# Kernel optimization log

Hardware: AMD Instinct MI355X
Metric: run time of the kernel (lower is better)

Reference implementation:

```python
import jax, jax.numpy as jnp
import numpy as np

D_MODEL = 1024
N_HEADS = 16
HEAD_DIM = D_MODEL // N_HEADS
SEQ_LEN = 2048
D_FF = 4 * D_MODEL
LCC_SCALE = 0.1
LN_EPS = 1e-5
NORM_EPS = 1e-12  # F.normalize eps


def _layer_norm(x, g, b):
    mu = jnp.mean(x, axis=-1, keepdims=True)
    var = jnp.mean(jnp.square(x - mu), axis=-1, keepdims=True)
    return (x - mu) * jax.lax.rsqrt(var + LN_EPS) * g + b


def setup_inputs() -> dict:
    key = jax.random.key(0)
    ks = jax.random.split(key, 8)
    s = 0.02  # weight init scale
    return {
        "x": jax.random.normal(ks[0], (SEQ_LEN, D_MODEL), jnp.float32),
        "lcc_values": jax.random.uniform(ks[1], (SEQ_LEN,), jnp.float32),
        "w_qkv": jax.random.normal(ks[2], (D_MODEL, 3 * D_MODEL), jnp.float32) * s,
        "b_qkv": jnp.zeros((3 * D_MODEL,), jnp.float32),
        "w_out": jax.random.normal(ks[3], (D_MODEL, D_MODEL), jnp.float32) * s,
        "b_out": jnp.zeros((D_MODEL,), jnp.float32),
        "ln1_g": jnp.ones((D_MODEL,), jnp.float32),
        "ln1_b": jnp.zeros((D_MODEL,), jnp.float32),
        "ln2_g": jnp.ones((D_MODEL,), jnp.float32),
        "ln2_b": jnp.zeros((D_MODEL,), jnp.float32),
        "w_ff1": jax.random.normal(ks[4], (D_MODEL, D_FF), jnp.float32) * s,
        "b_ff1": jnp.zeros((D_FF,), jnp.float32),
        "w_ff2": jax.random.normal(ks[5], (D_FF, D_MODEL), jnp.float32) * s,
        "b_ff2": jnp.zeros((D_MODEL,), jnp.float32),
    }


def reference(x, lcc_values, w_qkv, b_qkv, w_out, b_out, ln1_g, ln1_b,
              ln2_g, ln2_b, w_ff1, b_ff1, w_ff2, b_ff2):
    L = x.shape[0]
    scaling = HEAD_DIM ** -0.5

    normed = _layer_norm(x, ln1_g, ln1_b)
    qkv = normed @ w_qkv + b_qkv                      # [L, 3D]
    qkv = qkv.reshape(L, 3, N_HEADS, HEAD_DIM)
    q = jnp.transpose(qkv[:, 0], (1, 0, 2))           # [H, L, d]
    k = jnp.transpose(qkv[:, 1], (1, 0, 2))
    v = jnp.transpose(qkv[:, 2], (1, 0, 2))

    # cosine attention: L2-normalize q, k
    q = q / jnp.maximum(jnp.linalg.norm(q, axis=-1, keepdims=True), NORM_EPS)
    k = k / jnp.maximum(jnp.linalg.norm(k, axis=-1, keepdims=True), NORM_EPS)
    q = q * scaling

    scores = jnp.einsum('hld,hmd->hlm', q, k)         # [H, L, L]
    bias = (lcc_values[:, None] + lcc_values[None, :]) * 0.5 * LCC_SCALE
    scores = jnp.clip(scores + bias[None], -10.0, 10.0)
    probs = jax.nn.softmax(scores, axis=-1)

    attn = jnp.einsum('hlm,hmd->hld', probs, v)       # [H, L, d]
    attn = jnp.transpose(attn, (1, 0, 2)).reshape(L, D_MODEL)
    x = x + (attn @ w_out + b_out)

    normed2 = _layer_norm(x, ln2_g, ln2_b)
    h = jax.nn.gelu(normed2 @ w_ff1 + b_ff1, approximate=False)
    x = x + (h @ w_ff2 + b_ff2)
    return x
```

## Files before the change

### kernel.cpp

```cpp
#include <hip/hip_runtime.h>
#include <hip/hip_bf16.h>

#define D_MODEL 1024
#define SEQ 2048
#define NH 16
#define HD 64
#define DFF 4096

typedef __attribute__((ext_vector_type(8))) __bf16 bf16x8;
typedef __attribute__((ext_vector_type(4))) float f32x4;

__device__ __forceinline__ unsigned short f2bf(float f) {
    union { float f; unsigned u; } v; v.f = f;
    unsigned r = v.u + 0x7fffu + ((v.u >> 16) & 1u);
    return (unsigned short)(r >> 16);
}
__device__ __forceinline__ unsigned pack2(float a, float b) {
    return (unsigned)f2bf(a) | ((unsigned)f2bf(b) << 16);
}
__device__ __forceinline__ float bf2f(unsigned short u) {
    union { unsigned u; float f; } v; v.u = ((unsigned)u) << 16;
    return v.f;
}
__device__ __forceinline__ bf16x8 ld_frag(const unsigned short* p) {
    union { uint4 u; bf16x8 b; } c;
    c.u = *(const uint4*)p;
    return c.b;
}

typedef __attribute__((address_space(3))) unsigned lds_u32;
typedef const __attribute__((address_space(1))) unsigned glob_u32;
__device__ __forceinline__ void gl_lds16(const unsigned short* g, unsigned short* l) {
    __builtin_amdgcn_global_load_lds((glob_u32*)g, (lds_u32*)l, 16, 0, 0);
}

#define MFMA16(a,b,c) __builtin_amdgcn_mfma_f32_16x16x32_bf16(a,b,c,0,0,0)

__global__ __launch_bounds__(256) void wcast_all(const float* __restrict__ wq, const float* __restrict__ wo,
                                                 const float* __restrict__ wf1, const float* __restrict__ wf2,
                                                 unsigned short* __restrict__ oq, unsigned short* __restrict__ oo,
                                                 unsigned short* __restrict__ of1, unsigned short* __restrict__ of2) {
    __shared__ unsigned short lt[64][72];
    int id = blockIdx.x;
    const float* W; unsigned short* O; int K, N, nb, kb;
    if (id < 768)       { W = wq;  O = oq;  K = 1024; N = 3072; nb = id % 48; kb = id / 48; }
    else if (id < 1024) { id -= 768;  W = wo;  O = oo;  K = 1024; N = 1024; nb = id & 15; kb = id >> 4; }
    else if (id < 2048) { id -= 1024; W = wf1; O = of1; K = 1024; N = 4096; nb = id & 63; kb = id >> 6; }
    else                { id -= 2048; W = wf2; O = of2; K = 4096; N = 1024; nb = id & 15; kb = id >> 4; }
    int t = threadIdx.x;
    int r = t >> 2, c0 = (t & 3) << 4;
    const float* src = W + (size_t)(kb*64 + r) * N + nb*64 + c0;
    float4 f0 = ((const float4*)src)[0];
    float4 f1 = ((const float4*)src)[1];
    float4 f2 = ((const float4*)src)[2];
    float4 f3 = ((const float4*)src)[3];
    unsigned* dst = (unsigned*)&lt[r][c0];
    dst[0]=pack2(f0.x,f0.y); dst[1]=pack2(f0.z,f0.w);
    dst[2]=pack2(f1.x,f1.y); dst[3]=pack2(f1.z,f1.w);
    dst[4]=pack2(f2.x,f2.y); dst[5]=pack2(f2.z,f2.w);
    dst[6]=pack2(f3.x,f3.y); dst[7]=pack2(f3.z,f3.w);
    __syncthreads();
    int n_ = t >> 2, k0 = (t & 3) << 4;
    unsigned obuf[8];
#pragma unroll
    for (int i = 0; i < 8; i++)
        obuf[i] = (unsigned)lt[k0 + 2*i][n_] | ((unsigned)lt[k0 + 2*i + 1][n_] << 16);
    unsigned short* out = O + (size_t)(nb*64 + n_) * K + kb*64 + k0;
    ((uint4*)out)[0] = *(uint4*)&obuf[0];
    ((uint4*)out)[1] = *(uint4*)&obuf[4];
}

__global__ __launch_bounds__(256) void ln_kernel(const float* __restrict__ x,
                                                 const float* __restrict__ g,
                                                 const float* __restrict__ b,
                                                 unsigned short* __restrict__ out) {
    int row = blockIdx.x, t = threadIdx.x;
    float4 v = ((const float4*)(x + (size_t)row * D_MODEL))[t];
    float s  = v.x + v.y + v.z + v.w;
    float sq = v.x*v.x + v.y*v.y + v.z*v.z + v.w*v.w;
#pragma unroll
    for (int m = 1; m < 64; m <<= 1) { s += __shfl_xor(s, m, 64); sq += __shfl_xor(sq, m, 64); }
    __shared__ float ls[4], lq[4];
    int wave = t >> 6, lane = t & 63;
    if (lane == 0) { ls[wave] = s; lq[wave] = sq; }
    __syncthreads();
    s  = ls[0]+ls[1]+ls[2]+ls[3];
    sq = lq[0]+lq[1]+lq[2]+lq[3];
    float mu  = s * (1.0f / D_MODEL);
    float var = sq * (1.0f / D_MODEL) - mu * mu;
    float rs  = rsqrtf(var + 1e-5f);
    int c = t * 4;
    float y0 = (v.x - mu) * rs * g[c+0] + b[c+0];
    float y1 = (v.y - mu) * rs * g[c+1] + b[c+1];
    float y2 = (v.z - mu) * rs * g[c+2] + b[c+2];
    float y3 = (v.w - mu) * rs * g[c+3] + b[c+3];
    unsigned* o = (unsigned*)(out + (size_t)row * D_MODEL + c);
    o[0] = pack2(y0, y1); o[1] = pack2(y2, y3);
}

__global__ __launch_bounds__(256) void reduce_ln(const float* __restrict__ x,
                                                 const float* __restrict__ bout,
                                                 const unsigned short* __restrict__ parts,
                                                 const float* __restrict__ g,
                                                 const float* __restrict__ b,
                                                 float* __restrict__ x1,
                                                 unsigned short* __restrict__ x2n) {
    int row = blockIdx.x, t = threadIdx.x;
    int i = row * 256 + t;
    float4 v = ((const float4*)x)[i];
    float4 bb = ((const float4*)bout)[t];
    v.x += bb.x; v.y += bb.y; v.z += bb.z; v.w += bb.w;
#pragma unroll
    for (int p = 0; p < 4; p++) {
        ushort4 u = ((const ushort4*)(parts + (size_t)p * SEQ * D_MODEL))[i];
        v.x += bf2f(u.x); v.y += bf2f(u.y); v.z += bf2f(u.z); v.w += bf2f(u.w);
    }
    ((float4*)x1)[i] = v;
    float s  = v.x + v.y + v.z + v.w;
    float sq = v.x*v.x + v.y*v.y + v.z*v.z + v.w*v.w;
#pragma unroll
    for (int m = 1; m < 64; m <<= 1) { s += __shfl_xor(s, m, 64); sq += __shfl_xor(sq, m, 64); }
    __shared__ float ls[4], lq[4];
    int wave = t >> 6, lane = t & 63;
    if (lane == 0) { ls[wave] = s; lq[wave] = sq; }
    __syncthreads();
    s  = ls[0]+ls[1]+ls[2]+ls[3];
    sq = lq[0]+lq[1]+lq[2]+lq[3];
    float mu  = s * (1.0f / D_MODEL);
    float var = sq * (1.0f / D_MODEL) - mu * mu;
    float rs  = rsqrtf(var + 1e-5f);
    int c = t * 4;
    float y0 = (v.x - mu) * rs * g[c+0] + b[c+0];
    float y1 = (v.y - mu) * rs * g[c+1] + b[c+1];
    float y2 = (v.z - mu) * rs * g[c+2] + b[c+2];
    float y3 = (v.w - mu) * rs * g[c+3] + b[c+3];
    unsigned* o = (unsigned*)(x2n + (size_t)row * D_MODEL + c);
    o[0] = pack2(y0, y1); o[1] = pack2(y2, y3);
}

__global__ __launch_bounds__(256) void reduce_ff2(const float* __restrict__ res,
                                                  const float* __restrict__ bias,
                                                  const unsigned short* __restrict__ parts,
                                                  float* __restrict__ out) {
    int i = blockIdx.x * 256 + threadIdx.x;
    float4 r = ((const float4*)res)[i];
    float4 b = ((const float4*)bias)[i & (D_MODEL/4 - 1)];
    r.x += b.x; r.y += b.y; r.z += b.z; r.w += b.w;
#pragma unroll
    for (int p = 0; p < 4; p++) {
        ushort4 u = ((const ushort4*)(parts + (size_t)p * SEQ * D_MODEL))[i];
        r.x += bf2f(u.x); r.y += bf2f(u.y); r.z += bf2f(u.z); r.w += bf2f(u.w);
    }
    ((float4*)out)[i] = r;
}

#define BMf 128
#define BNf 256
#define FBUF_U16 ((BMf + BNf) * 64)
#define FSMEM_U16 (2 * FBUF_U16)
__device__ __forceinline__ void gemm_core_ff(const unsigned short* __restrict__ A,
                                             const unsigned short* __restrict__ Bt,
                                             int K, int K0, int KS, int bm, int bn,
                                             unsigned short* smem, f32x4 acc[4][4],
                                             int w, int lane) {
    int quad = lane >> 4, lr = lane & 15;
    int wm = w >> 2, wn = w & 3;
    const unsigned short* pa[2]; int da[2];
#pragma unroll
    for (int i = 0; i < 2; i++) {
        int rl = w*16 + i*8 + (lane >> 3);
        int sc = (lane & 7) ^ (rl & 7);
        pa[i] = A + (size_t)(bm*BMf + rl) * K + K0 + sc*8;
        da[i] = (w*16 + i*8) * 64;
    }
    const unsigned short* pb[4]; int db[4];
#pragma unroll
    for (int i = 0; i < 4; i++) {
        int rl = w*32 + i*8 + (lane >> 3);
        int sc = (lane & 7) ^ (rl & 7);
        pb[i] = Bt + (size_t)(bn*BNf + rl) * K + K0 + sc*8;
        db[i] = BMf*64 + (w*32 + i*8) * 64;
    }
    int foA[2][4], foB[2][4];
#pragma unroll
    for (int i = 0; i < 4; i++) {
        int ra = wm*64 + i*16 + lr;
        foA[0][i] = ra*64 + ((quad     ^ (ra & 7)))*8;
        foA[1][i] = ra*64 + (((quad+4) ^ (ra & 7)))*8;
        int rb = wn*64 + i*16 + lr;
        foB[0][i] = BMf*64 + rb*64 + ((quad     ^ (rb & 7)))*8;
        foB[1][i] = BMf*64 + rb*64 + (((quad+4) ^ (rb & 7)))*8;
    }
    int T = KS >> 6;
#pragma unroll
    for (int t = 0; t < 2; t++) {
        unsigned short* s = smem + t * FBUF_U16;
#pragma unroll
        for (int i = 0; i < 2; i++) gl_lds16(pa[i] + t*64, s + da[i]);
#pragma unroll
        for (int i = 0; i < 4; i++) gl_lds16(pb[i] + t*64, s + db[i]);
    }
    for (int t = 0; t < T; t++) {
        if (t + 1 < T) asm volatile("s_waitcnt vmcnt(6)" ::: "memory");
        else           asm volatile("s_waitcnt vmcnt(0)" ::: "memory");
        __builtin_amdgcn_s_barrier();
        const unsigned short* s = smem + (t & 1) * FBUF_U16;
#pragma unroll
        for (int h = 0; h < 2; h++) {
            bf16x8 af[4], bfr[4];
#pragma unroll
            for (int i = 0; i < 4; i++) af[i]  = ld_frag(s + foA[h][i]);
#pragma unroll
            for (int j = 0; j < 4; j++) bfr[j] = ld_frag(s + foB[h][j]);
            __builtin_amdgcn_s_setprio(1);
#pragma unroll
            for (int i = 0; i < 4; i++)
#pragma unroll
                for (int j = 0; j < 4; j++)
                    acc[i][j] = MFMA16(af[i], bfr[j], acc[i][j]);
            __builtin_amdgcn_s_setprio(0);
        }
        __builtin_amdgcn_s_barrier();
        if (t + 2 < T) {
            unsigned short* sn = smem + (t & 1) * FBUF_U16;
#pragma unroll
            for (int i = 0; i < 2; i++) gl_lds16(pa[i] + (t+2)*64, sn + da[i]);
#pragma unroll
            for (int i = 0; i < 4; i++) gl_lds16(pb[i] + (t+2)*64, sn + db[i]);
        }
    }
}

__device__ __forceinline__ void acc_init(f32x4 acc[4][4]) {
    f32x4 z = {0.f, 0.f, 0.f, 0.f};
#pragma unroll
    for (int i = 0; i < 4; i++)
#pragma unroll
        for (int j = 0; j < 4; j++) acc[i][j] = z;
}

__global__ __launch_bounds__(512, 2) void k_gemm_ff1(const unsigned short* __restrict__ A,
                                                     const unsigned short* __restrict__ Bt,
                                                     const float* __restrict__ bias,
                                                     unsigned short* __restrict__ C,
                                                     int M, int N, int K) {
    __shared__ unsigned short smem[FSMEM_U16];
    int t = threadIdx.x, w = t >> 6, lane = t & 63;
    int bn = blockIdx.x, bm = blockIdx.y;
    int quad = lane >> 4, lr = lane & 15;
    f32x4 acc[4][4];
    acc_init(acc);
    gemm_core_ff(A, Bt, K, 0, K, bm, bn, smem, acc, w, lane);
    int wm = w >> 2, wn = w & 3;
#pragma unroll
    for (int j = 0; j < 4; j++) {
        int col = bn*BNf + wn*64 + j*16 + lr;
        float bvv = bias[col];
#pragma unroll
        for (int i = 0; i < 4; i++) {
            int row0 = bm*BMf + wm*64 + i*16 + quad*4;
#pragma unroll
            for (int r = 0; r < 4; r++) {
                float v = acc[i][j][r] + bvv;
                v = 0.5f * v * (1.0f + erff(v * 0.70710678118654752f));
                C[(size_t)(row0 + r) * N + col] = f2bf(v);
            }
        }
    }
}

__global__ __launch_bounds__(512, 2) void k_gemm_ff2(const unsigned short* __restrict__ A,
                                                     const unsigned short* __restrict__ Bt,
                                                     unsigned short* __restrict__ C,
                                                     int M, int N, int K) {
    __shared__ unsigned short smem[FSMEM_U16];
    int t = threadIdx.x, w = t >> 6, lane = t & 63;
    int bn = blockIdx.x, bm = blockIdx.y, kz = blockIdx.z;
    int quad = lane >> 4, lr = lane & 15;
    int KS = K >> 2;
    f32x4 acc[4][4];
    acc_init(acc);
    gemm_core_ff(A, Bt, K, kz*KS, KS, bm, bn, smem, acc, w, lane);
    int wm = w >> 2, wn = w & 3;
    unsigned short* P = C + (size_t)kz * M * N;
#pragma unroll
    for (int j = 0; j < 4; j++) {
        int col = bn*BNf + wn*64 + j*16 + lr;
#pragma unroll
        for (int i = 0; i < 4; i++) {
            int row0 = bm*BMf + wm*64 + i*16 + quad*4;
#pragma unroll
            for (int r = 0; r < 4; r++)
                P[(size_t)(row0 + r) * N + col] = f2bf(acc[i][j][r]);
        }
    }
}

#define TMg 128
#define TNg 128
#define HALFg ((TMg + TNg) * 64)
#define SMEM_U16 (2 * HALFg)
__device__ __forceinline__ void gemm_core512(const unsigned short* __restrict__ A,
                                             const unsigned short* __restrict__ Bt,
                                             int K, int K0, int KS, int bm, int bn,
                                             unsigned short* smem, f32x4 acc[4][4],
                                             int w, int lane) {
    int quad = lane >> 4, lr = lane & 15;
    int kg = w >> 2;
    const unsigned short* pa[2]; const unsigned short* pb[2];
    int aoff[2], boff[2];
#pragma unroll
    for (int i = 0; i < 2; i++) {
        int rl = i*64 + w*8 + (lane >> 3);
        int sc = (lane & 7) ^ (rl & 7);
        pa[i] = A  + (size_t)(bm*TMg + rl) * K + K0 + sc*8;
        pb[i] = Bt + (size_t)(bn*TNg + rl) * K + K0 + sc*8;
        aoff[i] = (i*64 + w*8) * 64;
        boff[i] = TMg*64 + (i*64 + w*8) * 64;
    }
    int wr = ((w >> 1) & 1) * 64, wc = (w & 1) * 64;
    int foA[4], foB[4];
#pragma unroll
    for (int i = 0; i < 4; i++) {
        int ra = wr + i*16 + lr;
        foA[i] = ra*64 + (((quad + 4*kg) ^ (ra & 7)))*8;
        int rb = wc + i*16 + lr;
        foB[i] = TMg*64 + rb*64 + (((quad + 4*kg) ^ (rb & 7)))*8;
    }
#pragma unroll
    for (int i = 0; i < 2; i++) { gl_lds16(pa[i], smem + aoff[i]); gl_lds16(pb[i], smem + boff[i]); }
    int bo = 0;
    int T = KS >> 6;
    for (int t = 0; t < T; t++) {
        __syncthreads();
        if (t + 1 < T) {
            int nb = bo ^ HALFg;
#pragma unroll
            for (int i = 0; i < 2; i++) {
                gl_lds16(pa[i] + (t+1)*64, smem + nb + aoff[i]);
                gl_lds16(pb[i] + (t+1)*64, smem + nb + boff[i]);
            }
        }
        const unsigned short* s = smem + bo;
        bf16x8 af[4], bfr[4];
#pragma unroll
        for (int i = 0; i < 4; i++) af[i] = ld_frag(s + foA[i]);
#pragma unroll
        for (int j = 0; j < 4; j++) bfr[j] = ld_frag(s + foB[j]);
        __builtin_amdgcn_s_setprio(1);
#pragma unroll
        for (int i = 0; i < 4; i++)
#pragma unroll
            for (int j = 0; j < 4; j++)
                acc[i][j] = MFMA16(af[i], bfr[j], acc[i][j]);
        __builtin_amdgcn_s_setprio(0);
        bo ^= HALFg;
    }
}

__device__ __forceinline__ void acc_merge_split(unsigned short* smem, f32x4 acc[4][4],
                                                int w, int lane) {
    float* X = (float*)smem;
    int kg = w >> 2, p = w & 3, quad = lane >> 4, lr = lane & 15;
    if (kg) {
#pragma unroll
        for (int i = 0; i < 4; i++) {
            f32x4 t0 = acc[i][0]; acc[i][0] = acc[i][2]; acc[i][2] = t0;
            f32x4 t1 = acc[i][1]; acc[i][1] = acc[i][3]; acc[i][3] = t1;
        }
    }
    __syncthreads();
    int g = (kg ^ 1) * 2;
#pragma unroll
    for (int i = 0; i < 4; i++)
#pragma unroll
        for (int r = 0; r < 4; r++) {
            int ro = (i*16 + r*4 + quad)*16 + lr;
            X[(p*4 + g    )*1024 + ro] = acc[i][2][r];
            X[(p*4 + g + 1)*1024 + ro] = acc[i][3][r];
        }
    __syncthreads();
    int k = kg * 2;
#pragma unroll
    for (int i = 0; i < 4; i++)
#pragma unroll
        for (int r = 0; r < 4; r++) {
            int ro = (i*16 + r*4 + quad)*16 + lr;
            acc[i][0][r] += X[(p*4 + k    )*1024 + ro];
            acc[i][1][r] += X[(p*4 + k + 1)*1024 + ro];
        }
}

__global__ __launch_bounds__(512, 4) void k_gemm_qkv(const unsigned short* __restrict__ A,
                                                     const unsigned short* __restrict__ Bt,
                                                     const float* __restrict__ bias,
                                                     unsigned short* __restrict__ qn,
                                                     unsigned short* __restrict__ kn,
                                                     unsigned short* __restrict__ vt) {
    __shared__ unsigned short smem[SMEM_U16];
    int t = threadIdx.x;
    int bn = blockIdx.x, bm = blockIdx.y;
    int w = t >> 6, lane = t & 63;
    int quad = lane >> 4, lr = lane & 15;
    f32x4 acc[4][4];
    acc_init(acc);
    gemm_core512(A, Bt, 1024, 0, 1024, bm, bn, smem, acc, w, lane);

    float* X = (float*)smem;
    int kg = w >> 2, p = w & 3;
    __syncthreads();
    if (kg == 1) {
#pragma unroll
        for (int j = 0; j < 4; j++) {
            float* slot = X + (p*4 + j)*1024;
#pragma unroll
            for (int i = 0; i < 4; i++)
#pragma unroll
                for (int r = 0; r < 4; r++)
                    slot[(i*16 + r*4 + quad)*16 + lr] = acc[i][j][r];
        }
    }
    __syncthreads();
    int wr = ((w >> 1) & 1) * 64, wc = (w & 1) * 64;
    int sec = bn >> 3, hp = bn & 7;
    if (kg == 0) {
#pragma unroll
        for (int j = 0; j < 4; j++) {
            const float* slot = X + (p*4 + j)*1024;
            float bv = bias[bn*TNg + wc + j*16 + lr];
#pragma unroll
            for (int i = 0; i < 4; i++)
#pragma unroll
                for (int r = 0; r < 4; r++)
                    acc[i][j][r] += slot[(i*16 + r*4 + quad)*16 + lr] + bv;
        }
    }

    if (sec < 2) {
        if (kg == 0) {
            int h = hp*2 + (w & 1);
            unsigned short* dst = (sec == 0) ? qn : kn;
            float mul = (sec == 0) ? 0.125f : 1.0f;
#pragma unroll
            for (int i = 0; i < 4; i++)
#pragma unroll
                for (int r = 0; r < 4; r++) {
                    float ss = 0.f;
#pragma unroll
                    for (int j = 0; j < 4; j++) ss += acc[i][j][r]*acc[i][j][r];
                    ss += __shfl_xor(ss, 1, 64); ss += __shfl_xor(ss, 2, 64);
                    ss += __shfl_xor(ss, 4, 64); ss += __shfl_xor(ss, 8, 64);
                    float scale = mul / fmaxf(sqrtf(ss), 1e-12f);
                    int row = bm*TMg + wr + i*16 + quad*4 + r;
                    size_t base = ((size_t)h*SEQ + row) * HD;
#pragma unroll
                    for (int j = 0; j < 4; j++)
                        dst[base + j*16 + lr] = f2bf(acc[i][j][r] * scale);
                }
        }
    } else {
        __syncthreads();
        unsigned short (*lv)[136] = (unsigned short (*)[136])smem;
        if (kg == 0) {
#pragma unroll
            for (int i = 0; i < 4; i++)
#pragma unroll
                for (int j = 0; j < 4; j++)
#pragma unroll
                    for (int r = 0; r < 4; r++)
                        lv[wc + j*16 + lr][wr + i*16 + quad*4 + r] = f2bf(acc[i][j][r]);
        }
        __syncthreads();
        int d = t >> 2, l0 = (t & 3) * 32;
        unsigned short* ov = vt + ((size_t)(hp*128 + d)) * SEQ + bm*TMg + l0;
#pragma unroll
        for (int c = 0; c < 4; c++)
            ((uint4*)ov)[c] = *(uint4*)&lv[d][l0 + c*8];
    }
}

template<int SPLITK>
__device__ __forceinline__ void gemm_part512(const unsigned short* A, const unsigned short* Bt,
                                             unsigned short* C, int M, int N, int K) {
    __shared__ unsigned short smem[SMEM_U16];
    int t = threadIdx.x;
    int bn = blockIdx.x, bm = blockIdx.y, kz = blockIdx.z;
    int w = t >> 6, lane = t & 63;
    int quad = lane >> 4, lr = lane & 15;
    int KS = K / SPLITK;
    f32x4 acc[4][4];
    acc_init(acc);
    gemm_core512(A, Bt, K, kz*KS, KS, bm, bn, smem, acc, w, lane);
    acc_merge_split(smem, acc, w, lane);
    int kg = w >> 2, wr = ((w >> 1) & 1) * 64, wc = (w & 1) * 64;
    unsigned short* P = C + (size_t)kz * M * N;
    int col0 = bn*TNg + wc + (kg*2)*16 + lr;
    int col1 = col0 + 16;
#pragma unroll
    for (int i = 0; i < 4; i++) {
        int row0 = bm*TMg + wr + i*16 + quad*4;
#pragma unroll
        for (int r = 0; r < 4; r++) {
            P[(size_t)(row0 + r) * N + col0] = f2bf(acc[i][0][r]);
            P[(size_t)(row0 + r) * N + col1] = f2bf(acc[i][1][r]);
        }
    }
}
__global__ __launch_bounds__(512, 4) void k_gemm_op(const unsigned short* A, const unsigned short* Bt,
                                                    unsigned short* C, int M, int N, int K) {
    gemm_part512<4>(A, Bt, C, M, N, K);
}

#define KSPLIT 2
#define KTILES (SEQ / 64 / KSPLIT)
__global__ __launch_bounds__(256) void attn_kernel(const unsigned short* __restrict__ qn,
                                                   const unsigned short* __restrict__ kn,
                                                   const unsigned short* __restrict__ vt,
                                                   const float* __restrict__ lcc,
                                                   float* __restrict__ num_ws,
                                                   float* __restrict__ den_ws) {
    __shared__ unsigned short lQP[64*64];
    __shared__ unsigned short lK[2][64*64];
    __shared__ unsigned short lV[2][64*64];
    int h = blockIdx.x, qb = blockIdx.y, kz = blockIdx.z;
    int t = threadIdx.x;
    int wave = t >> 6, lane = t & 63, quad = lane >> 4, lr = lane & 15;
    int r0 = lane >> 3;
    int ch = lane & 7;

    const unsigned short* kn0 = kn + (size_t)h*SEQ*HD + (size_t)kz*(SEQ/KSPLIT)*HD;
    const unsigned short* vt0 = vt + (size_t)h*HD*SEQ + kz*(SEQ/KSPLIT);
    const float* lcc0 = lcc + kz*(SEQ/KSPLIT);

#pragma unroll
    for (int i = 0; i < 2; i++) {
        int rl = wave*16 + i*8 + r0;
        int ss = ch ^ (rl & 7);
        gl_lds16(qn + ((size_t)h*SEQ + qb*64 + rl)*HD + ss*8, lQP + (wave*16 + i*8)*64);
        gl_lds16(kn0 + (size_t)rl*HD + ss*8,                  lK[0] + (wave*16 + i*8)*64);
        gl_lds16(vt0 + (size_t)rl*SEQ + ss*8,                 lV[0] + (wave*16 + i*8)*64);
    }
    __syncthreads();

    bf16x8 aq0 = ld_frag(lQP + (wave*16 + lr)*64 + ((quad     ^ (lr & 7)))*8);
    bf16x8 aq1 = ld_frag(lQP + (wave*16 + lr)*64 + (((quad+4) ^ (lr & 7)))*8);

    f32x4 z = {0.f, 0.f, 0.f, 0.f};
    f32x4 oacc[4]; oacc[0]=z; oacc[1]=z; oacc[2]=z; oacc[3]=z;
    float den[4] = {0.f, 0.f, 0.f, 0.f};

    int cur = 0;
    for (int kb = 0; kb < KTILES; kb++) {
        if (kb + 1 < KTILES) {
            int nxt = cur ^ 1;
#pragma unroll
            for (int i = 0; i < 2; i++) {
                int rl = wave*16 + i*8 + r0;
                int ss = ch ^ (rl & 7);
                gl_lds16(kn0 + (size_t)(kb+1)*64*HD + (size_t)rl*HD + ss*8,
                         lK[nxt] + (wave*16 + i*8)*64);
                gl_lds16(vt0 + (size_t)rl*SEQ + (kb+1)*64 + ss*8,
                         lV[nxt] + (wave*16 + i*8)*64);
            }
        }
        float lmv[4];
#pragma unroll
        for (int j = 0; j < 4; j++) lmv[j] = 0.05f * lcc0[kb*64 + j*16 + lr];

        __builtin_amdgcn_s_setprio(1);
        const unsigned short* Kc = lK[cur];
#pragma unroll
        for (int j = 0; j < 4; j++) {
            bf16x8 b0 = ld_frag(Kc + (j*16 + lr)*64 + ((quad     ^ (lr & 7)))*8);
            bf16x8 b1 = ld_frag(Kc + (j*16 + lr)*64 + (((quad+4) ^ (lr & 7)))*8);
            f32x4 s = z;
            s = MFMA16(aq0, b0, s);
            s = MFMA16(aq1, b1, s);
#pragma unroll
            for (int r = 0; r < 4; r++) {
                float p = __expf(s[r] + lmv[j]);
                den[r] += p;
                int prow = wave*16 + quad*4 + r;
                lQP[prow*64 + (((2*j + (lr >> 3)) ^ (prow & 7)))*8 + (lr & 7)] = f2bf(p);
            }
        }
        bf16x8 ap0 = ld_frag(lQP + (wave*16 + lr)*64 + ((quad     ^ (lr & 7)))*8);
        bf16x8 ap1 = ld_frag(lQP + (wave*16 + lr)*64 + (((quad+4) ^ (lr & 7)))*8);
        const unsigned short* Vc = lV[cur];
#pragma unroll
        for (int j2 = 0; j2 < 4; j2++) {
            bf16x8 b0 = ld_frag(Vc + (j2*16 + lr)*64 + ((quad     ^ (lr & 7)))*8);
            bf16x8 b1 = ld_frag(Vc + (j2*16 + lr)*64 + (((quad+4) ^ (lr & 7)))*8);
            oacc[j2] = MFMA16(ap0, b0, oacc[j2]);
            oacc[j2] = MFMA16(ap1, b1, oacc[j2]);
        }
        __builtin_amdgcn_s_setprio(0);
        __syncthreads();
        cur ^= 1;
    }
#pragma unroll
    for (int r = 0; r < 4; r++)
#pragma unroll
        for (int m = 1; m < 16; m <<= 1) den[r] += __shfl_xor(den[r], m, 64);

    float* nump = num_ws + (((size_t)(h*32 + qb)) * KSPLIT + kz) * 4096;
#pragma unroll
    for (int j2 = 0; j2 < 4; j2++)
#pragma unroll
        for (int r = 0; r < 4; r++)
            nump[(wave*16 + quad*4 + r) * 64 + j2*16 + lr] = oacc[j2][r];
    if (lr == 0) {
        float* denp = den_ws + (((size_t)(h*32 + qb)) * KSPLIT + kz) * 64;
#pragma unroll
        for (int r = 0; r < 4; r++) denp[wave*16 + quad*4 + r] = den[r];
    }
}

__global__ __launch_bounds__(256) void attn_comb(const float* __restrict__ num_ws,
                                                 const float* __restrict__ den_ws,
                                                 unsigned short* __restrict__ attn) {
    int hq = blockIdx.x;
    int h = hq >> 5, qb = hq & 31;
    int t = threadIdx.x;
    int row = t >> 2, col0 = (t & 3) << 4;
    const float* n0 = num_ws + ((size_t)hq * KSPLIT) * 4096 + row*64 + col0;
    const float* n1 = n0 + 4096;
    float d = den_ws[(size_t)hq * KSPLIT * 64 + row] + den_ws[((size_t)hq * KSPLIT + 1) * 64 + row];
    float inv = 1.0f / d;
    unsigned ob[8];
#pragma unroll
    for (int i = 0; i < 4; i++) {
        float4 a = ((const float4*)n0)[i];
        float4 b = ((const float4*)n1)[i];
        ob[2*i]   = pack2((a.x + b.x) * inv, (a.y + b.y) * inv);
        ob[2*i+1] = pack2((a.z + b.z) * inv, (a.w + b.w) * inv);
    }
    unsigned short* op = attn + (size_t)(qb*64 + row) * D_MODEL + h*64 + col0;
    ((uint4*)op)[0] = *(uint4*)&ob[0];
    ((uint4*)op)[1] = *(uint4*)&ob[4];
}

extern "C" void kernel_launch(void* const* d_in, const int* in_sizes, int n_in,
                              void* d_out, int out_size, void* d_ws, size_t ws_size,
                              hipStream_t stream) {
    const float* x      = (const float*)d_in[0];
    const float* lcc    = (const float*)d_in[1];
    const float* w_qkv  = (const float*)d_in[2];
    const float* b_qkv  = (const float*)d_in[3];
    const float* w_out  = (const float*)d_in[4];
    const float* b_out  = (const float*)d_in[5];
    const float* ln1_g  = (const float*)d_in[6];
    const float* ln1_b  = (const float*)d_in[7];
    const float* ln2_g  = (const float*)d_in[8];
    const float* ln2_b  = (const float*)d_in[9];
    const float* w_ff1  = (const float*)d_in[10];
    const float* b_ff1  = (const float*)d_in[11];
    const float* w_ff2  = (const float*)d_in[12];
    const float* b_ff2  = (const float*)d_in[13];

    char* ws = (char*)d_ws;
    unsigned short* wtq  = (unsigned short*)(ws);
    unsigned short* wto  = (unsigned short*)(ws + 6291456);
    unsigned short* wtf1 = (unsigned short*)(ws + 8388608);
    unsigned short* wtf2 = (unsigned short*)(ws + 16777216);
    unsigned short* xn   = (unsigned short*)(ws + 25165824);
    float*          x1   = (float*)(ws + 29360128);
    float*          numw = (float*)(ws + 29360128);
    float*          denw = (float*)(ws + 46137344);
    unsigned short* hbuf = (unsigned short*)(ws + 37748736);
    unsigned short* pOP  = (unsigned short*)(ws + 37748736);
    unsigned short* qnb  = (unsigned short*)(ws + 54525952);
    unsigned short* knb  = (unsigned short*)(ws + 58720256);
    unsigned short* vtb  = (unsigned short*)(ws + 62914560);
    unsigned short* pFF2 = (unsigned short*)(ws);
    unsigned short* attnb = xn;
    unsigned short* x2n  = qnb;
    float* outp = (float*)d_out;


    wcast_all<<<3072, 256, 0, stream>>>(w_qkv, w_out, w_ff1, w_ff2, wtq, wto, wtf1, wtf2);
    ln_kernel<<<SEQ, 256, 0, stream>>>(x, ln1_g, ln1_b, xn);
    k_gemm_qkv<<<dim3(24, 16), 512, 0, stream>>>(xn, wtq, b_qkv, qnb, knb, vtb);
    attn_kernel<<<dim3(16, 32, KSPLIT), 256, 0, stream>>>(qnb, knb, vtb, lcc, numw, denw);
    attn_comb<<<512, 256, 0, stream>>>(numw, denw, attnb);
    k_gemm_op<<<dim3(8, 16, 4), 512, 0, stream>>>(attnb, wto, pOP, SEQ, 1024, 1024);
    reduce_ln<<<SEQ, 256, 0, stream>>>(x, b_out, pOP, ln2_g, ln2_b, x1, x2n);
    k_gemm_ff1<<<dim3(16, 16), 512, 0, stream>>>(x2n, wtf1, b_ff1, hbuf, SEQ, 4096, 1024);
    k_gemm_ff2<<<dim3(4, 16, 4), 512, 0, stream>>>(hbuf, wtf2, pFF2, SEQ, 1024, 4096);
    reduce_ff2<<<SEQ*D_MODEL/1024, 256, 0, stream>>>(x1, b_ff2, pFF2, outp);
}
```

Baseline: 257.0 us.

## Move QKV and out-proj GEMMs onto the larger 128x256 ff GEMM core

Replaces the 128x128 in-block split-K GEMM core, which merged partial sums through LDS, with the wider gemm_core_ff tile already used for the FF GEMMs, applied to both the QKV and out-projection GEMMs. The QKV epilogue is rewritten for the new warp layout, with one head per wave column for the q/k normalization and a 256-column V transpose through LDS. This cuts the grid sizes in half and removes the LDS reduction step. In exchange there are fewer blocks, 192 and 256, to fill the CUs, and occupancy is lower (2 blocks per CU instead of 4).

```diff
diff --git a/kernel.cpp b/kernel.cpp
--- a/kernel.cpp
+++ b/kernel.cpp
@@ -239,6 +239,97 @@
         for (int j = 0; j < 4; j++) acc[i][j] = z;
 }
 
+__global__ __launch_bounds__(512, 2) void k_gemm_qkv(const unsigned short* __restrict__ A,
+                                                     const unsigned short* __restrict__ Bt,
+                                                     const float* __restrict__ bias,
+                                                     unsigned short* __restrict__ qn,
+                                                     unsigned short* __restrict__ kn,
+                                                     unsigned short* __restrict__ vt) {
+    __shared__ unsigned short smem[FSMEM_U16];
+    int t = threadIdx.x, w = t >> 6, lane = t & 63;
+    int bn = blockIdx.x, bm = blockIdx.y;
+    int quad = lane >> 4, lr = lane & 15;
+    f32x4 acc[4][4];
+    acc_init(acc);
+    gemm_core_ff(A, Bt, 1024, 0, 1024, bm, bn, smem, acc, w, lane);
+
+    int wm = w >> 2, wn = w & 3;
+    int sec = bn >> 2;
+#pragma unroll
+    for (int j = 0; j < 4; j++) {
+        float bv = bias[bn*BNf + wn*64 + j*16 + lr];
+#pragma unroll
+        for (int i = 0; i < 4; i++)
+#pragma unroll
+            for (int r = 0; r < 4; r++) acc[i][j][r] += bv;
+    }
+
+    if (sec < 2) {
+        int h = (bn & 3)*4 + wn;
+        unsigned short* dst = (sec == 0) ? qn : kn;
+        float mul = (sec == 0) ? 0.125f : 1.0f;
+#pragma unroll
+        for (int i = 0; i < 4; i++)
+#pragma unroll
+            for (int r = 0; r < 4; r++) {
+                float ss = 0.f;
+#pragma unroll
+                for (int j = 0; j < 4; j++) ss += acc[i][j][r]*acc[i][j][r];
+                ss += __shfl_xor(ss, 1, 64); ss += __shfl_xor(ss, 2, 64);
+                ss += __shfl_xor(ss, 4, 64); ss += __shfl_xor(ss, 8, 64);
+                float scale = mul / fmaxf(sqrtf(ss), 1e-12f);
+                int row = bm*BMf + wm*64 + i*16 + quad*4 + r;
+                size_t base = ((size_t)h*SEQ + row) * HD;
+#pragma unroll
+                for (int j = 0; j < 4; j++)
+                    dst[base + j*16 + lr] = f2bf(acc[i][j][r] * scale);
+            }
+    } else {
+        __syncthreads();
+        unsigned short (*lv)[136] = (unsigned short (*)[136])smem;
+#pragma unroll
+        for (int i = 0; i < 4; i++)
+#pragma unroll
+            for (int j = 0; j < 4; j++)
+#pragma unroll
+                for (int r = 0; r < 4; r++)
+                    lv[wn*64 + j*16 + lr][wm*64 + i*16 + quad*4 + r] = f2bf(acc[i][j][r]);
+        __syncthreads();
+        int c = t >> 1, l0 = (t & 1) * 64;
+        unsigned short* ov = vt + ((size_t)((bn - 8)*256 + c)) * SEQ + bm*BMf + l0;
+#pragma unroll
+        for (int q = 0; q < 8; q++)
+            ((uint4*)ov)[q] = *(uint4*)&lv[c][l0 + q*8];
+    }
+}
+
+__global__ __launch_bounds__(512, 2) void k_gemm_op(const unsigned short* __restrict__ A,
+                                                    const unsigned short* __restrict__ Bt,
+                                                    unsigned short* __restrict__ C,
+                                                    int M, int N, int K) {
+    __shared__ unsigned short smem[FSMEM_U16];
+    int t = threadIdx.x, w = t >> 6, lane = t & 63;
+    int bn = blockIdx.x, bm = blockIdx.y, kz = blockIdx.z;
+    int quad = lane >> 4, lr = lane & 15;
+    int KS = K >> 2;
+    f32x4 acc[4][4];
+    acc_init(acc);
+    gemm_core_ff(A, Bt, K, kz*KS, KS, bm, bn, smem, acc, w, lane);
+    int wm = w >> 2, wn = w & 3;
+    unsigned short* P = C + (size_t)kz * M * N;
+#pragma unroll
+    for (int j = 0; j < 4; j++) {
+        int col = bn*BNf + wn*64 + j*16 + lr;
+#pragma unroll
+        for (int i = 0; i < 4; i++) {
+            int row0 = bm*BMf + wm*64 + i*16 + quad*4;
+#pragma unroll
+            for (int r = 0; r < 4; r++)
+                P[(size_t)(row0 + r) * N + col] = f2bf(acc[i][j][r]);
+        }
+    }
+}
+
 __global__ __launch_bounds__(512, 2) void k_gemm_ff1(const unsigned short* __restrict__ A,
                                                      const unsigned short* __restrict__ Bt,
                                                      const float* __restrict__ bias,
@@ -294,221 +385,6 @@
                 P[(size_t)(row0 + r) * N + col] = f2bf(acc[i][j][r]);
         }
     }
-}
-
-#define TMg 128
-#define TNg 128
-#define HALFg ((TMg + TNg) * 64)
-#define SMEM_U16 (2 * HALFg)
-__device__ __forceinline__ void gemm_core512(const unsigned short* __restrict__ A,
-                                             const unsigned short* __restrict__ Bt,
-                                             int K, int K0, int KS, int bm, int bn,
-                                             unsigned short* smem, f32x4 acc[4][4],
-                                             int w, int lane) {
-    int quad = lane >> 4, lr = lane & 15;
-    int kg = w >> 2;
-    const unsigned short* pa[2]; const unsigned short* pb[2];
-    int aoff[2], boff[2];
-#pragma unroll
-    for (int i = 0; i < 2; i++) {
-        int rl = i*64 + w*8 + (lane >> 3);
-        int sc = (lane & 7) ^ (rl & 7);
-        pa[i] = A  + (size_t)(bm*TMg + rl) * K + K0 + sc*8;
-        pb[i] = Bt + (size_t)(bn*TNg + rl) * K + K0 + sc*8;
-        aoff[i] = (i*64 + w*8) * 64;
-        boff[i] = TMg*64 + (i*64 + w*8) * 64;
-    }
-    int wr = ((w >> 1) & 1) * 64, wc = (w & 1) * 64;
-    int foA[4], foB[4];
-#pragma unroll
-    for (int i = 0; i < 4; i++) {
-        int ra = wr + i*16 + lr;
-        foA[i] = ra*64 + (((quad + 4*kg) ^ (ra & 7)))*8;
-        int rb = wc + i*16 + lr;
-        foB[i] = TMg*64 + rb*64 + (((quad + 4*kg) ^ (rb & 7)))*8;
-    }
-#pragma unroll
-    for (int i = 0; i < 2; i++) { gl_lds16(pa[i], smem + aoff[i]); gl_lds16(pb[i], smem + boff[i]); }
-    int bo = 0;
-    int T = KS >> 6;
-    for (int t = 0; t < T; t++) {
-        __syncthreads();
-        if (t + 1 < T) {
-            int nb = bo ^ HALFg;
-#pragma unroll
-            for (int i = 0; i < 2; i++) {
-                gl_lds16(pa[i] + (t+1)*64, smem + nb + aoff[i]);
-                gl_lds16(pb[i] + (t+1)*64, smem + nb + boff[i]);
-            }
-        }
-        const unsigned short* s = smem + bo;
-        bf16x8 af[4], bfr[4];
-#pragma unroll
-        for (int i = 0; i < 4; i++) af[i] = ld_frag(s + foA[i]);
-#pragma unroll
-        for (int j = 0; j < 4; j++) bfr[j] = ld_frag(s + foB[j]);
-        __builtin_amdgcn_s_setprio(1);
-#pragma unroll
-        for (int i = 0; i < 4; i++)
-#pragma unroll
-            for (int j = 0; j < 4; j++)
-                acc[i][j] = MFMA16(af[i], bfr[j], acc[i][j]);
-        __builtin_amdgcn_s_setprio(0);
-        bo ^= HALFg;
-    }
-}
-
-__device__ __forceinline__ void acc_merge_split(unsigned short* smem, f32x4 acc[4][4],
-                                                int w, int lane) {
-    float* X = (float*)smem;
-    int kg = w >> 2, p = w & 3, quad = lane >> 4, lr = lane & 15;
-    if (kg) {
-#pragma unroll
-        for (int i = 0; i < 4; i++) {
-            f32x4 t0 = acc[i][0]; acc[i][0] = acc[i][2]; acc[i][2] = t0;
-            f32x4 t1 = acc[i][1]; acc[i][1] = acc[i][3]; acc[i][3] = t1;
-        }
-    }
-    __syncthreads();
-    int g = (kg ^ 1) * 2;
-#pragma unroll
-    for (int i = 0; i < 4; i++)
-#pragma unroll
-        for (int r = 0; r < 4; r++) {
-            int ro = (i*16 + r*4 + quad)*16 + lr;
-            X[(p*4 + g    )*1024 + ro] = acc[i][2][r];
-            X[(p*4 + g + 1)*1024 + ro] = acc[i][3][r];
-        }
-    __syncthreads();
-    int k = kg * 2;
-#pragma unroll
-    for (int i = 0; i < 4; i++)
-#pragma unroll
-        for (int r = 0; r < 4; r++) {
-            int ro = (i*16 + r*4 + quad)*16 + lr;
-            acc[i][0][r] += X[(p*4 + k    )*1024 + ro];
-            acc[i][1][r] += X[(p*4 + k + 1)*1024 + ro];
-        }
-}
-
-__global__ __launch_bounds__(512, 4) void k_gemm_qkv(const unsigned short* __restrict__ A,
-                                                     const unsigned short* __restrict__ Bt,
-                                                     const float* __restrict__ bias,
-                                                     unsigned short* __restrict__ qn,
-                                                     unsigned short* __restrict__ kn,
-                                                     unsigned short* __restrict__ vt) {
-    __shared__ unsigned short smem[SMEM_U16];
-    int t = threadIdx.x;
-    int bn = blockIdx.x, bm = blockIdx.y;
-    int w = t >> 6, lane = t & 63;
-    int quad = lane >> 4, lr = lane & 15;
-    f32x4 acc[4][4];
-    acc_init(acc);
-    gemm_core512(A, Bt, 1024, 0, 1024, bm, bn, smem, acc, w, lane);
-
-    float* X = (float*)smem;
-    int kg = w >> 2, p = w & 3;
-    __syncthreads();
-    if (kg == 1) {
-#pragma unroll
-        for (int j = 0; j < 4; j++) {
-            float* slot = X + (p*4 + j)*1024;
-#pragma unroll
-            for (int i = 0; i < 4; i++)
-#pragma unroll
-                for (int r = 0; r < 4; r++)
-                    slot[(i*16 + r*4 + quad)*16 + lr] = acc[i][j][r];
-        }
-    }
-    __syncthreads();
-    int wr = ((w >> 1) & 1) * 64, wc = (w & 1) * 64;
-    int sec = bn >> 3, hp = bn & 7;
-    if (kg == 0) {
-#pragma unroll
-        for (int j = 0; j < 4; j++) {
-            const float* slot = X + (p*4 + j)*1024;
-            float bv = bias[bn*TNg + wc + j*16 + lr];
-#pragma unroll
-            for (int i = 0; i < 4; i++)
-#pragma unroll
-                for (int r = 0; r < 4; r++)
-                    acc[i][j][r] += slot[(i*16 + r*4 + quad)*16 + lr] + bv;
-        }
-    }
-
-    if (sec < 2) {
-        if (kg == 0) {
-            int h = hp*2 + (w & 1);
-            unsigned short* dst = (sec == 0) ? qn : kn;
-            float mul = (sec == 0) ? 0.125f : 1.0f;
-#pragma unroll
-            for (int i = 0; i < 4; i++)
-#pragma unroll
-                for (int r = 0; r < 4; r++) {
-                    float ss = 0.f;
-#pragma unroll
-                    for (int j = 0; j < 4; j++) ss += acc[i][j][r]*acc[i][j][r];
-                    ss += __shfl_xor(ss, 1, 64); ss += __shfl_xor(ss, 2, 64);
-                    ss += __shfl_xor(ss, 4, 64); ss += __shfl_xor(ss, 8, 64);
-                    float scale = mul / fmaxf(sqrtf(ss), 1e-12f);
-                    int row = bm*TMg + wr + i*16 + quad*4 + r;
-                    size_t base = ((size_t)h*SEQ + row) * HD;
-#pragma unroll
-                    for (int j = 0; j < 4; j++)
-                        dst[base + j*16 + lr] = f2bf(acc[i][j][r] * scale);
-                }
-        }
-    } else {
-        __syncthreads();
-        unsigned short (*lv)[136] = (unsigned short (*)[136])smem;
-        if (kg == 0) {
-#pragma unroll
-            for (int i = 0; i < 4; i++)
-#pragma unroll
-                for (int j = 0; j < 4; j++)
-#pragma unroll
-                    for (int r = 0; r < 4; r++)
-                        lv[wc + j*16 + lr][wr + i*16 + quad*4 + r] = f2bf(acc[i][j][r]);
-        }
-        __syncthreads();
-        int d = t >> 2, l0 = (t & 3) * 32;
-        unsigned short* ov = vt + ((size_t)(hp*128 + d)) * SEQ + bm*TMg + l0;
-#pragma unroll
-        for (int c = 0; c < 4; c++)
-            ((uint4*)ov)[c] = *(uint4*)&lv[d][l0 + c*8];
-    }
-}
-
-template<int SPLITK>
-__device__ __forceinline__ void gemm_part512(const unsigned short* A, const unsigned short* Bt,
-                                             unsigned short* C, int M, int N, int K) {
-    __shared__ unsigned short smem[SMEM_U16];
-    int t = threadIdx.x;
-    int bn = blockIdx.x, bm = blockIdx.y, kz = blockIdx.z;
-    int w = t >> 6, lane = t & 63;
-    int quad = lane >> 4, lr = lane & 15;
-    int KS = K / SPLITK;
-    f32x4 acc[4][4];
-    acc_init(acc);
-    gemm_core512(A, Bt, K, kz*KS, KS, bm, bn, smem, acc, w, lane);
-    acc_merge_split(smem, acc, w, lane);
-    int kg = w >> 2, wr = ((w >> 1) & 1) * 64, wc = (w & 1) * 64;
-    unsigned short* P = C + (size_t)kz * M * N;
-    int col0 = bn*TNg + wc + (kg*2)*16 + lr;
-    int col1 = col0 + 16;
-#pragma unroll
-    for (int i = 0; i < 4; i++) {
-        int row0 = bm*TMg + wr + i*16 + quad*4;
-#pragma unroll
-        for (int r = 0; r < 4; r++) {
-            P[(size_t)(row0 + r) * N + col0] = f2bf(acc[i][0][r]);
-            P[(size_t)(row0 + r) * N + col1] = f2bf(acc[i][1][r]);
-        }
-    }
-}
-__global__ __launch_bounds__(512, 4) void k_gemm_op(const unsigned short* A, const unsigned short* Bt,
-                                                    unsigned short* C, int M, int N, int K) {
-    gemm_part512<4>(A, Bt, C, M, N, K);
 }
 
 #define KSPLIT 2
@@ -680,10 +556,10 @@
 
     wcast_all<<<3072, 256, 0, stream>>>(w_qkv, w_out, w_ff1, w_ff2, wtq, wto, wtf1, wtf2);
     ln_kernel<<<SEQ, 256, 0, stream>>>(x, ln1_g, ln1_b, xn);
-    k_gemm_qkv<<<dim3(24, 16), 512, 0, stream>>>(xn, wtq, b_qkv, qnb, knb, vtb);
+    k_gemm_qkv<<<dim3(12, 16), 512, 0, stream>>>(xn, wtq, b_qkv, qnb, knb, vtb);
     attn_kernel<<<dim3(16, 32, KSPLIT), 256, 0, stream>>>(qnb, knb, vtb, lcc, numw, denw);
     attn_comb<<<512, 256, 0, stream>>>(numw, denw, attnb);
-    k_gemm_op<<<dim3(8, 16, 4), 512, 0, stream>>>(attnb, wto, pOP, SEQ, 1024, 1024);
+    k_gemm_op<<<dim3(4, 16, 4), 512, 0, stream>>>(attnb, wto, pOP, SEQ, 1024, 1024);
     reduce_ln<<<SEQ, 256, 0, stream>>>(x, b_out, pOP, ln2_g, ln2_b, x1, x2n);
     k_gemm_ff1<<<dim3(16, 16), 512, 0, stream>>>(x2n, wtf1, b_ff1, hbuf, SEQ, 4096, 1024);
     k_gemm_ff2<<<dim3(4, 16, 4), 512, 0, stream>>>(hbuf, wtf2, pFF2, SEQ, 1024, 4096);
```

Measured after the change: 261.2 us. No clear change (+1.6%).
